# Kernel optimization log

Hardware: AMD Instinct MI355X
Metric: run time of the kernel (lower is better)

## Reference

```python
import jax, jax.numpy as jnp
import numpy as np

EPS = 1e-5  # torch LayerNorm default


def setup_inputs() -> dict:
    key = jax.random.key(0)
    ks = jax.random.split(key, 4)
    B, S, D = 8, 1024, 768
    return {
        "q": jax.random.normal(ks[0], (B, S, D), dtype=jnp.float32),
        "k": jax.random.normal(ks[1], (B, S, D), dtype=jnp.float32),
        "v": jax.random.normal(ks[2], (B, S, D), dtype=jnp.float32),
        "W": jax.random.normal(ks[3], (D, D), dtype=jnp.float32) * (1.0 / np.sqrt(D)),
        "gamma": jnp.ones((D,), dtype=jnp.float32),
        "beta": jnp.zeros((D,), dtype=jnp.float32),
        "n_heads": 12,
    }


def reference(q, k, v, W, gamma, beta, n_heads):
    # Shapes: q,k,v [B,S,D]; W [D,D] (torch Linear weight, y = x @ W.T)
    B, S, D = q.shape
    Dh = D // n_heads

    proj = lambda x: jax.nn.relu(x @ W.T)
    q1, k1, v1 = proj(q), proj(k), proj(v)

    # chunk(dim=2) + cat(dim=0) == reshape to per-head [B,S,H,Dh]
    split = lambda x: x.reshape(B, S, n_heads, Dh)
    qh, kh, vh = split(q1), split(k1), split(v1)

    scale = 1.0 / (Dh ** 0.5)
    scores = jnp.einsum("bqhd,bkhd->bhqk", qh, kh) * scale  # [B,H,S,S]
    attn = jax.nn.softmax(scores, axis=-1)  # dropout is identity in eval mode
    out = jnp.einsum("bhqk,bkhd->bqhd", attn, vh).reshape(B, S, D)

    # `outputs += outputs + q` in torch -> outputs = 2*outputs + q
    out = 2.0 * out + q

    mu = jnp.mean(out, axis=-1, keepdims=True)
    var = jnp.var(out, axis=-1, keepdims=True)
    return (out - mu) / jnp.sqrt(var + EPS) * gamma + beta
```

## Files before the change

kernel.cpp:

```cpp
#include <hip/hip_runtime.h>
#include <hip/hip_bf16.h>

#define B_  8
#define S_  1024
#define D_  768
#define H_  12
#define DH_ 64

typedef __attribute__((ext_vector_type(8))) short bf16x8;
typedef __attribute__((ext_vector_type(4))) float f32x4;
typedef __attribute__((ext_vector_type(16))) float f32x16;

__device__ inline short f2bf(float f) {
    unsigned u = __builtin_bit_cast(unsigned, f);
    u = (u + 0x7fffu + ((u >> 16) & 1u)) >> 16;
    return (short)u;
}
__device__ inline float exp2_fast(float x) {
    float r; asm("v_exp_f32 %0, %1" : "=v"(r) : "v"(x)); return r;
}
__device__ inline unsigned cvt_pk_bf16(float lo, float hi) {
    unsigned r; asm("v_cvt_pk_bf16_f32 %0, %1, %2" : "=v"(r) : "v"(lo), "v"(hi)); return r;
}
__device__ inline float rcp_fast(float x) {
    float r; asm("v_rcp_f32 %0, %1" : "=v"(r) : "v"(x)); return r;
}
__device__ inline void plswap(unsigned& a, unsigned& b) {
    auto r = __builtin_amdgcn_permlane32_swap(a, b, false, false);
    a = r[0]; b = r[1];
}
__device__ inline float2 xhalves(float x) {
    unsigned u = __builtin_bit_cast(unsigned, x);
    auto r = __builtin_amdgcn_permlane32_swap(u, u, false, false);
    return make_float2(__builtin_bit_cast(float, r[0]),
                       __builtin_bit_cast(float, r[1]));
}

__global__ __launch_bounds__(256) void proj_kernel(
    const float* __restrict__ q, const float* __restrict__ k,
    const float* __restrict__ v, const float* __restrict__ W,
    short* __restrict__ q1, short* __restrict__ k1, short* __restrict__ v1t)
{
    __shared__ __align__(16) char lds_raw[36864];
    short (*As)[72]  = reinterpret_cast<short(*)[72]>(lds_raw);
    short (*Bs)[72]  = reinterpret_cast<short(*)[72]>(lds_raw + 18432);
    short (*Ts)[136] = reinterpret_cast<short(*)[136]>(lds_raw);

    int p  = blockIdx.x;
    int L  = (p & 7) * 144 + (p >> 3);
    int mt = L / 6, nt = L % 6;
    int t  = mt >> 6;
    int m0 = (mt & 63) << 7;
    int n0 = nt << 7;
    const float* X = (t == 0) ? q : (t == 1) ? k : v;

    int tid  = threadIdx.x;
    int lane = tid & 63;
    int w    = tid >> 6;
    int wr   = w >> 1, wc = w & 1;
    int l15  = lane & 15;
    int g    = lane >> 4;

    int srow = tid >> 4;
    int scol = (tid & 15) << 2;

    const float* ax = X + (size_t)(m0 + srow) * D_ + scol;
    const float* bx = W + (size_t)(n0 + srow) * D_ + scol;

    f32x4 acc[4][4];
    #pragma unroll
    for (int m = 0; m < 4; m++)
        #pragma unroll
        for (int n = 0; n < 4; n++) acc[m][n] = (f32x4){0.f, 0.f, 0.f, 0.f};

    f32x4 la[8], lb[8];
    #pragma unroll
    for (int r = 0; r < 8; r++) {
        la[r] = *(const f32x4*)(ax + r * 16 * D_);
        lb[r] = *(const f32x4*)(bx + r * 16 * D_);
    }

    for (int kb = 0; kb < D_; kb += 64) {
        asm volatile("" ::: "memory");
        __builtin_amdgcn_s_barrier();
        asm volatile("" ::: "memory");
        #pragma unroll
        for (int r = 0; r < 8; r++) {
            uint2 ua, ub;
            ua.x = cvt_pk_bf16(la[r][0], la[r][1]);
            ua.y = cvt_pk_bf16(la[r][2], la[r][3]);
            ub.x = cvt_pk_bf16(lb[r][0], lb[r][1]);
            ub.y = cvt_pk_bf16(lb[r][2], lb[r][3]);
            *(uint2*)&As[r * 16 + srow][scol] = ua;
            *(uint2*)&Bs[r * 16 + srow][scol] = ub;
        }
        if (kb + 64 < D_) {
            #pragma unroll
            for (int r = 0; r < 8; r++) {
                la[r] = *(const f32x4*)(ax + kb + 64 + r * 16 * D_);
                lb[r] = *(const f32x4*)(bx + kb + 64 + r * 16 * D_);
            }
        }
        asm volatile("s_waitcnt lgkmcnt(0)" ::: "memory");
        __builtin_amdgcn_s_barrier();
        __builtin_amdgcn_sched_barrier(0);
        #pragma unroll
        for (int kk = 0; kk < 2; kk++) {
            int c = kk * 32 + (g << 3);
            bf16x8 af[4], bfv[4];
            #pragma unroll
            for (int m = 0; m < 4; m++)
                af[m] = *(const bf16x8*)&As[wr * 64 + m * 16 + l15][c];
            #pragma unroll
            for (int n = 0; n < 4; n++)
                bfv[n] = *(const bf16x8*)&Bs[wc * 64 + n * 16 + l15][c];
            #pragma unroll
            for (int m = 0; m < 4; m++)
                #pragma unroll
                for (int n = 0; n < 4; n++)
                    acc[m][n] = __builtin_amdgcn_mfma_f32_16x16x32_bf16(
                        af[m], bfv[n], acc[m][n], 0, 0, 0);
        }
    }

    __syncthreads();
    const float sc1 = (t == 1) ? 0.18033688011112793f : 1.0f;
    #pragma unroll
    for (int m = 0; m < 4; m++) {
        int rb = wr * 64 + m * 16 + (g << 2);
        #pragma unroll
        for (int n = 0; n < 4; n++) {
            int cb = wc * 64 + n * 16 + l15;
            #pragma unroll
            for (int r = 0; r < 4; r++) {
                short vv = f2bf(fmaxf(acc[m][n][r], 0.f) * sc1);
                if (t == 2) Ts[cb][rb + r] = vv;
                else        Ts[rb + r][cb] = vv;
            }
        }
    }
    __syncthreads();
    int row = tid >> 1;
    int c0  = (tid & 1) << 6;
    if (t == 2) {
        int gc = n0 + row;
        int h = gc >> 6, dh = gc & 63;
        int bb = m0 >> 10, s0 = m0 & 1023;
        short* dst = v1t + (((size_t)bb * H_ + h) * DH_ + dh) * S_ + s0 + c0;
        #pragma unroll
        for (int j = 0; j < 8; j++)
            *(bf16x8*)(dst + j * 8) = *(const bf16x8*)&Ts[row][c0 + j * 8];
    } else {
        int m = m0 + row;
        int bb = m >> 10, ss = m & 1023;
        int h = (n0 >> 6) + (tid & 1);
        short* dst = (t ? k1 : q1) + (((size_t)bb * H_ + h) * S_ + ss) * DH_;
        #pragma unroll
        for (int j = 0; j < 8; j++)
            *(bf16x8*)(dst + j * 8) = *(const bf16x8*)&Ts[row][c0 + j * 8];
    }
}

__global__ __launch_bounds__(256, 3) void attn_kernel(
    const short* __restrict__ q1, const short* __restrict__ k1,
    const short* __restrict__ v1t, float* __restrict__ out)
{
    __shared__ short Klds[2][4096];
    __shared__ short Vlds[2][4096];
    __shared__ float lsum_lds[4][32];

    int d    = blockIdx.x;
    int head = (d & 7) + ((d >> 6) << 3);
    int qi   = (d >> 3) & 7;
    int bb   = head / H_, hh = head % H_;

    int tid = threadIdx.x, lane = tid & 63, w = tid >> 6;
    int l31 = lane & 31, hi = lane >> 5;
    int qbase = (qi * 4 + w) * 32;

    const short* Qp = q1  + (size_t)head * S_ * DH_;
    const short* Kp = k1  + (size_t)head * S_ * DH_;
    const short* Vp = v1t + (size_t)head * DH_ * S_;

    int sr = tid >> 2, sc = tid & 3;
    int swz0 = sr * 128 + ((sc       ^ (sr & 7)) << 4);
    int swz1 = sr * 128 + (((sc + 4) ^ (sr & 7)) << 4);

    bf16x8 stK0, stK1, stV0, stV1;

#define LOADST(kvb) do { \
        const short* _kg = Kp + (size_t)((kvb) + sr) * DH_; \
        const short* _vg = Vp + (size_t)sr * S_ + (kvb); \
        stK0 = *(const bf16x8*)(_kg + sc * 8); \
        stK1 = *(const bf16x8*)(_kg + (sc + 4) * 8); \
        stV0 = *(const bf16x8*)(_vg + sc * 8); \
        stV1 = *(const bf16x8*)(_vg + (sc + 4) * 8); \
    } while (0)
#define WRITEST(buf) do { \
        char* _kb = (char*)&Klds[buf][0]; \
        char* _vb = (char*)&Vlds[buf][0]; \
        *(bf16x8*)(_kb + swz0) = stK0; \
        *(bf16x8*)(_kb + swz1) = stK1; \
        *(bf16x8*)(_vb + swz0) = stV0; \
        *(bf16x8*)(_vb + swz1) = stV1; \
    } while (0)

    bf16x8 qf[4];
    #pragma unroll
    for (int kb = 0; kb < 4; kb++)
        qf[kb] = *(const bf16x8*)(Qp + (size_t)(qbase + l31) * DH_ + kb * 16 + hi * 8);

    f32x16 o0, o1;
    #pragma unroll
    for (int r = 0; r < 16; r++) { o0[r] = 0.f; o1[r] = 0.f; }
    float mreg = -1e30f, lsum = 0.f;

    int xk = l31 & 7;

    auto subtile = [&](int cur, int j) {
        const char* Kt = (const char*)&Klds[cur][0];
        const char* Vt = (const char*)&Vlds[cur][0];
        int rK = (32 * j + l31) * 128;
        bf16x8 kf0 = *(const bf16x8*)(Kt + rK + (((0 + hi) ^ xk) << 4));
        bf16x8 kf1 = *(const bf16x8*)(Kt + rK + (((2 + hi) ^ xk) << 4));
        bf16x8 kf2 = *(const bf16x8*)(Kt + rK + (((4 + hi) ^ xk) << 4));
        bf16x8 kf3 = *(const bf16x8*)(Kt + rK + (((6 + hi) ^ xk) << 4));
        int rV0 = l31 * 128, rV1 = (32 + l31) * 128;
        int s0 = ((4 * j + hi) ^ xk) << 4, s1 = ((4 * j + 2 + hi) ^ xk) << 4;
        bf16x8 vf00 = *(const bf16x8*)(Vt + rV0 + s0);
        bf16x8 vf01 = *(const bf16x8*)(Vt + rV0 + s1);
        bf16x8 vf10 = *(const bf16x8*)(Vt + rV1 + s0);
        bf16x8 vf11 = *(const bf16x8*)(Vt + rV1 + s1);

        f32x16 s;
        #pragma unroll
        for (int r = 0; r < 16; r++) s[r] = 0.f;
        __builtin_amdgcn_s_setprio(1);
        s = __builtin_amdgcn_mfma_f32_32x32x16_bf16(kf0, qf[0], s, 0, 0, 0);
        s = __builtin_amdgcn_mfma_f32_32x32x16_bf16(kf1, qf[1], s, 0, 0, 0);
        s = __builtin_amdgcn_mfma_f32_32x32x16_bf16(kf2, qf[2], s, 0, 0, 0);
        s = __builtin_amdgcn_mfma_f32_32x32x16_bf16(kf3, qf[3], s, 0, 0, 0);
        __builtin_amdgcn_s_setprio(0);

        float t0 = fmaxf(s[0], s[1]),   t1 = fmaxf(s[2], s[3]);
        float t2 = fmaxf(s[4], s[5]),   t3 = fmaxf(s[6], s[7]);
        float t4 = fmaxf(s[8], s[9]),   t5 = fmaxf(s[10], s[11]);
        float t6 = fmaxf(s[12], s[13]), t7 = fmaxf(s[14], s[15]);
        float u0 = fmaxf(t0, t1), u1 = fmaxf(t2, t3);
        float u2 = fmaxf(t4, t5), u3 = fmaxf(t6, t7);
        float pmax = fmaxf(fmaxf(u0, u1), fmaxf(u2, u3));
        float2 ph = xhalves(pmax);
        pmax = fmaxf(ph.x, ph.y);

        if (!__all(pmax <= mreg + 8.f)) {
            float mn = fmaxf(mreg, pmax);
            float sc_ = exp2_fast(mreg - mn);
            mreg = mn; lsum *= sc_;
            if (hi == 0) lsum_lds[w][l31] = sc_;
            asm volatile("s_waitcnt lgkmcnt(0)" ::: "memory");
            #pragma unroll
            for (int r = 0; r < 16; r++) {
                int crow = (r & 3) + ((r >> 2) << 3) + (hi << 2);
                float srw = lsum_lds[w][crow];
                o0[r] *= srw; o1[r] *= srw;
            }
        }

        #pragma unroll
        for (int r = 0; r < 16; r++) s[r] = exp2_fast(s[r] - mreg);

        float a0 = s[0] + s[1],   a1 = s[2] + s[3];
        float a2 = s[4] + s[5],   a3 = s[6] + s[7];
        float a4 = s[8] + s[9],   a5 = s[10] + s[11];
        float a6 = s[12] + s[13], a7 = s[14] + s[15];
        float rsum = ((a0 + a1) + (a2 + a3)) + ((a4 + a5) + (a6 + a7));
        float2 rh = xhalves(rsum);
        lsum += rh.x + rh.y;

        unsigned c0 = cvt_pk_bf16(s[0], s[1]);
        unsigned c1 = cvt_pk_bf16(s[2], s[3]);
        unsigned c2 = cvt_pk_bf16(s[4], s[5]);
        unsigned c3 = cvt_pk_bf16(s[6], s[7]);
        unsigned c4 = cvt_pk_bf16(s[8], s[9]);
        unsigned c5 = cvt_pk_bf16(s[10], s[11]);
        unsigned c6 = cvt_pk_bf16(s[12], s[13]);
        unsigned c7 = cvt_pk_bf16(s[14], s[15]);
        plswap(c0, c2);
        plswap(c1, c3);
        plswap(c4, c6);
        plswap(c5, c7);

        union U { unsigned u[4]; bf16x8 v; };
        U f0, f1;
        f0.u[0] = c0; f0.u[1] = c1; f0.u[2] = c2; f0.u[3] = c3;
        f1.u[0] = c4; f1.u[1] = c5; f1.u[2] = c6; f1.u[3] = c7;

        __builtin_amdgcn_s_setprio(1);
        o0 = __builtin_amdgcn_mfma_f32_32x32x16_bf16(f0.v, vf00, o0, 0, 0, 0);
        o0 = __builtin_amdgcn_mfma_f32_32x32x16_bf16(f1.v, vf01, o0, 0, 0, 0);
        o1 = __builtin_amdgcn_mfma_f32_32x32x16_bf16(f0.v, vf10, o1, 0, 0, 0);
        o1 = __builtin_amdgcn_mfma_f32_32x32x16_bf16(f1.v, vf11, o1, 0, 0, 0);
        __builtin_amdgcn_s_setprio(0);
    };

    LOADST(0);
    WRITEST(0);
    LOADST(64);
    asm volatile("s_waitcnt lgkmcnt(0)" ::: "memory");
    __builtin_amdgcn_s_barrier();
    asm volatile("" ::: "memory");

    int cur = 0;
    for (int t = 0; t < 16; t++) {
        if (t < 15) {
            WRITEST(cur ^ 1);
            if (t < 14) LOADST((t + 2) * 64);
        }
        subtile(cur, 0);
        subtile(cur, 1);
        if (t < 15) {
            asm volatile("" ::: "memory");
            asm volatile("s_waitcnt lgkmcnt(0)" ::: "memory");
            __builtin_amdgcn_s_barrier();
            asm volatile("" ::: "memory");
        }
        cur ^= 1;
    }
#undef LOADST
#undef WRITEST

    if (hi == 0) lsum_lds[w][l31] = lsum;
    asm volatile("s_waitcnt lgkmcnt(0)" ::: "memory");
    #pragma unroll
    for (int r = 0; r < 16; r++) {
        int crow = (r & 3) + ((r >> 2) << 3) + (hi << 2);
        float inv = rcp_fast(lsum_lds[w][crow]);
        float* op = out + ((size_t)(bb * S_ + qbase + crow)) * D_ + hh * DH_ + l31;
        op[0]  = o0[r] * inv;
        op[32] = o1[r] * inv;
    }
}

__global__ __launch_bounds__(192) void ln_kernel(
    const float* __restrict__ qin, const float* __restrict__ gamma,
    const float* __restrict__ beta, float* __restrict__ out)
{
    int row = blockIdx.x;
    int tid = threadIdx.x;
    size_t base = (size_t)row * D_ + tid * 4;

    f32x4 o  = *(const f32x4*)(out + base);
    f32x4 qv = *(const f32x4*)(qin + base);
    f32x4 x;
    float sum = 0.f, sq = 0.f;
    #pragma unroll
    for (int i = 0; i < 4; i++) {
        x[i] = 2.f * o[i] + qv[i];
        sum += x[i];
        sq  += x[i] * x[i];
    }
    #pragma unroll
    for (int msk = 1; msk < 64; msk <<= 1) {
        sum += __shfl_xor(sum, msk);
        sq  += __shfl_xor(sq, msk);
    }
    __shared__ float s1[3], s2[3];
    if ((tid & 63) == 0) { s1[tid >> 6] = sum; s2[tid >> 6] = sq; }
    __syncthreads();
    sum = s1[0] + s1[1] + s1[2];
    sq  = s2[0] + s2[1] + s2[2];
    float mu   = sum * (1.f / D_);
    float var  = sq * (1.f / D_) - mu * mu;
    float rstd = rsqrtf(var + 1e-5f);
    f32x4 g = *(const f32x4*)(gamma + tid * 4);
    f32x4 b = *(const f32x4*)(beta + tid * 4);
    f32x4 y;
    #pragma unroll
    for (int i = 0; i < 4; i++)
        y[i] = (x[i] - mu) * rstd * g[i] + b[i];
    *(f32x4*)(out + base) = y;
}

extern "C" void kernel_launch(void* const* d_in, const int* in_sizes, int n_in,
                              void* d_out, int out_size, void* d_ws, size_t ws_size,
                              hipStream_t stream)
{
    const float* q     = (const float*)d_in[0];
    const float* k     = (const float*)d_in[1];
    const float* v     = (const float*)d_in[2];
    const float* W     = (const float*)d_in[3];
    const float* gamma = (const float*)d_in[4];
    const float* beta  = (const float*)d_in[5];

    size_t per = (size_t)B_ * H_ * S_ * DH_;
    short* q1  = (short*)d_ws;
    short* k1  = q1 + per;
    short* v1t = k1 + per;
    float* out = (float*)d_out;

    proj_kernel<<<dim3(1152), dim3(256), 0, stream>>>(q, k, v, W, q1, k1, v1t);
    attn_kernel<<<dim3(768), dim3(256), 0, stream>>>(q1, k1, v1t, out);
    ln_kernel<<<dim3(B_ * S_), dim3(192), 0, stream>>>(q, gamma, beta, out);
}
```

Measured before the change: 120.7 us.

## Double-buffer projection GEMM LDS with XOR swizzle and finer K steps

Restructures the projection GEMM main loop into a double-buffered LDS pipeline over 32-wide K steps, so each iteration needs one barrier instead of two and the global loads run two steps ahead. Padded LDS rows are replaced with XOR-swizzled layouts for the A/B tiles and the epilogue transpose buffer to avoid bank conflicts, and total LDS drops to 32KB. The launch bound now asks for 4 blocks per CU, and MFMA sections get raised wave priority. The risks are register pressure from the occupancy hint and shallower per-step MFMA work relative to barrier overhead.

```diff
diff --git a/kernel.cpp b/kernel.cpp
--- a/kernel.cpp
+++ b/kernel.cpp
@@ -36,15 +36,12 @@
                        __builtin_bit_cast(float, r[1]));
 }
 
-__global__ __launch_bounds__(256) void proj_kernel(
+__global__ __launch_bounds__(256, 4) void proj_kernel(
     const float* __restrict__ q, const float* __restrict__ k,
     const float* __restrict__ v, const float* __restrict__ W,
     short* __restrict__ q1, short* __restrict__ k1, short* __restrict__ v1t)
 {
-    __shared__ __align__(16) char lds_raw[36864];
-    short (*As)[72]  = reinterpret_cast<short(*)[72]>(lds_raw);
-    short (*Bs)[72]  = reinterpret_cast<short(*)[72]>(lds_raw + 18432);
-    short (*Ts)[136] = reinterpret_cast<short(*)[136]>(lds_raw);
+    __shared__ __align__(16) char lds_raw[32768];
 
     int p  = blockIdx.x;
     int L  = (p & 7) * 144 + (p >> 3);
@@ -54,18 +51,40 @@
     int n0 = nt << 7;
     const float* X = (t == 0) ? q : (t == 1) ? k : v;
 
-    int tid  = threadIdx.x;
-    int lane = tid & 63;
-    int w    = tid >> 6;
-    int wr   = w >> 1, wc = w & 1;
-    int l15  = lane & 15;
-    int g    = lane >> 4;
-
-    int srow = tid >> 4;
-    int scol = (tid & 15) << 2;
-
-    const float* ax = X + (size_t)(m0 + srow) * D_ + scol;
-    const float* bx = W + (size_t)(n0 + srow) * D_ + scol;
+    int tid = threadIdx.x, lane = tid & 63, w = tid >> 6;
+    int wr = w >> 1, wc = w & 1;
+    int l15 = lane & 15, g = lane >> 4;
+
+    int srow = tid >> 1, h = tid & 1;
+    const float* ax = X + (size_t)(m0 + srow) * D_ + h * 16;
+    const float* bx = W + (size_t)(n0 + srow) * D_ + h * 16;
+
+    int wb0 = srow * 64 + ((((h << 1) | 0) ^ (srow & 3)) << 4);
+    int wb1 = srow * 64 + ((((h << 1) | 1) ^ (srow & 3)) << 4);
+    int fs = (g ^ (l15 & 3)) << 4;
+
+    f32x4 la[4], lb[4];
+#define LOADAB(step) do { int _c = (step) * 32; \
+        la[0] = *(const f32x4*)(ax + _c);      la[1] = *(const f32x4*)(ax + _c + 4); \
+        la[2] = *(const f32x4*)(ax + _c + 8);  la[3] = *(const f32x4*)(ax + _c + 12); \
+        lb[0] = *(const f32x4*)(bx + _c);      lb[1] = *(const f32x4*)(bx + _c + 4); \
+        lb[2] = *(const f32x4*)(bx + _c + 8);  lb[3] = *(const f32x4*)(bx + _c + 12); \
+    } while (0)
+#define CONVW(bufbase) do { \
+        uint4 ua0, ua1, ub0, ub1; \
+        ua0.x = cvt_pk_bf16(la[0][0], la[0][1]); ua0.y = cvt_pk_bf16(la[0][2], la[0][3]); \
+        ua0.z = cvt_pk_bf16(la[1][0], la[1][1]); ua0.w = cvt_pk_bf16(la[1][2], la[1][3]); \
+        ua1.x = cvt_pk_bf16(la[2][0], la[2][1]); ua1.y = cvt_pk_bf16(la[2][2], la[2][3]); \
+        ua1.z = cvt_pk_bf16(la[3][0], la[3][1]); ua1.w = cvt_pk_bf16(la[3][2], la[3][3]); \
+        ub0.x = cvt_pk_bf16(lb[0][0], lb[0][1]); ub0.y = cvt_pk_bf16(lb[0][2], lb[0][3]); \
+        ub0.z = cvt_pk_bf16(lb[1][0], lb[1][1]); ub0.w = cvt_pk_bf16(lb[1][2], lb[1][3]); \
+        ub1.x = cvt_pk_bf16(lb[2][0], lb[2][1]); ub1.y = cvt_pk_bf16(lb[2][2], lb[2][3]); \
+        ub1.z = cvt_pk_bf16(lb[3][0], lb[3][1]); ub1.w = cvt_pk_bf16(lb[3][2], lb[3][3]); \
+        *(uint4*)(lds_raw + (bufbase) + wb0)        = ua0; \
+        *(uint4*)(lds_raw + (bufbase) + wb1)        = ua1; \
+        *(uint4*)(lds_raw + (bufbase) + 8192 + wb0) = ub0; \
+        *(uint4*)(lds_raw + (bufbase) + 8192 + wb1) = ub1; \
+    } while (0)
 
     f32x4 acc[4][4];
     #pragma unroll
@@ -73,55 +92,41 @@
         #pragma unroll
         for (int n = 0; n < 4; n++) acc[m][n] = (f32x4){0.f, 0.f, 0.f, 0.f};
 
-    f32x4 la[8], lb[8];
-    #pragma unroll
-    for (int r = 0; r < 8; r++) {
-        la[r] = *(const f32x4*)(ax + r * 16 * D_);
-        lb[r] = *(const f32x4*)(bx + r * 16 * D_);
-    }
-
-    for (int kb = 0; kb < D_; kb += 64) {
-        asm volatile("" ::: "memory");
-        __builtin_amdgcn_s_barrier();
-        asm volatile("" ::: "memory");
-        #pragma unroll
-        for (int r = 0; r < 8; r++) {
-            uint2 ua, ub;
-            ua.x = cvt_pk_bf16(la[r][0], la[r][1]);
-            ua.y = cvt_pk_bf16(la[r][2], la[r][3]);
-            ub.x = cvt_pk_bf16(lb[r][0], lb[r][1]);
-            ub.y = cvt_pk_bf16(lb[r][2], lb[r][3]);
-            *(uint2*)&As[r * 16 + srow][scol] = ua;
-            *(uint2*)&Bs[r * 16 + srow][scol] = ub;
-        }
-        if (kb + 64 < D_) {
-            #pragma unroll
-            for (int r = 0; r < 8; r++) {
-                la[r] = *(const f32x4*)(ax + kb + 64 + r * 16 * D_);
-                lb[r] = *(const f32x4*)(bx + kb + 64 + r * 16 * D_);
-            }
-        }
-        asm volatile("s_waitcnt lgkmcnt(0)" ::: "memory");
-        __builtin_amdgcn_s_barrier();
-        __builtin_amdgcn_sched_barrier(0);
-        #pragma unroll
-        for (int kk = 0; kk < 2; kk++) {
-            int c = kk * 32 + (g << 3);
-            bf16x8 af[4], bfv[4];
-            #pragma unroll
-            for (int m = 0; m < 4; m++)
-                af[m] = *(const bf16x8*)&As[wr * 64 + m * 16 + l15][c];
+    LOADAB(0);
+    CONVW(0);
+    LOADAB(1);
+    asm volatile("s_waitcnt lgkmcnt(0)" ::: "memory");
+    __builtin_amdgcn_s_barrier();
+    asm volatile("" ::: "memory");
+
+    #pragma unroll 2
+    for (int s = 0; s < 24; ++s) {
+        if (s < 23) CONVW(((s + 1) & 1) << 14);
+        if (s < 22) LOADAB(s + 2);
+        const char* bufp = lds_raw + ((s & 1) << 14);
+        bf16x8 af[4], bfv[4];
+        #pragma unroll
+        for (int m = 0; m < 4; m++)
+            af[m] = *(const bf16x8*)(bufp + (wr * 64 + m * 16 + l15) * 64 + fs);
+        #pragma unroll
+        for (int n = 0; n < 4; n++)
+            bfv[n] = *(const bf16x8*)(bufp + 8192 + (wc * 64 + n * 16 + l15) * 64 + fs);
+        __builtin_amdgcn_s_setprio(1);
+        #pragma unroll
+        for (int m = 0; m < 4; m++)
             #pragma unroll
             for (int n = 0; n < 4; n++)
-                bfv[n] = *(const bf16x8*)&Bs[wc * 64 + n * 16 + l15][c];
-            #pragma unroll
-            for (int m = 0; m < 4; m++)
-                #pragma unroll
-                for (int n = 0; n < 4; n++)
-                    acc[m][n] = __builtin_amdgcn_mfma_f32_16x16x32_bf16(
-                        af[m], bfv[n], acc[m][n], 0, 0, 0);
+                acc[m][n] = __builtin_amdgcn_mfma_f32_16x16x32_bf16(
+                    af[m], bfv[n], acc[m][n], 0, 0, 0);
+        __builtin_amdgcn_s_setprio(0);
+        if (s < 23) {
+            asm volatile("s_waitcnt lgkmcnt(0)" ::: "memory");
+            __builtin_amdgcn_s_barrier();
+            asm volatile("" ::: "memory");
         }
     }
+#undef LOADAB
+#undef CONVW
 
     __syncthreads();
     const float sc1 = (t == 1) ? 0.18033688011112793f : 1.0f;
@@ -134,30 +139,35 @@
             #pragma unroll
             for (int r = 0; r < 4; r++) {
                 short vv = f2bf(fmaxf(acc[m][n][r], 0.f) * sc1);
-                if (t == 2) Ts[cb][rb + r] = vv;
-                else        Ts[rb + r][cb] = vv;
+                int rr = (t == 2) ? cb : rb + r;
+                int cc = (t == 2) ? rb + r : cb;
+                *(short*)(lds_raw + rr * 256 + (((cc >> 3) ^ (rr & 15)) << 4)
+                          + ((cc & 7) << 1)) = vv;
             }
         }
     }
     __syncthreads();
     int row = tid >> 1;
     int c0  = (tid & 1) << 6;
+    bf16x8 ov[8];
+    #pragma unroll
+    for (int j = 0; j < 8; j++)
+        ov[j] = *(const bf16x8*)(lds_raw + row * 256 +
+                 ((((c0 >> 3) + j) ^ (row & 15)) << 4));
     if (t == 2) {
         int gc = n0 + row;
-        int h = gc >> 6, dh = gc & 63;
+        int hh2 = gc >> 6, dh = gc & 63;
         int bb = m0 >> 10, s0 = m0 & 1023;
-        short* dst = v1t + (((size_t)bb * H_ + h) * DH_ + dh) * S_ + s0 + c0;
-        #pragma unroll
-        for (int j = 0; j < 8; j++)
-            *(bf16x8*)(dst + j * 8) = *(const bf16x8*)&Ts[row][c0 + j * 8];
+        short* dst = v1t + (((size_t)bb * H_ + hh2) * DH_ + dh) * S_ + s0 + c0;
+        #pragma unroll
+        for (int j = 0; j < 8; j++) *(bf16x8*)(dst + j * 8) = ov[j];
     } else {
         int m = m0 + row;
         int bb = m >> 10, ss = m & 1023;
-        int h = (n0 >> 6) + (tid & 1);
-        short* dst = (t ? k1 : q1) + (((size_t)bb * H_ + h) * S_ + ss) * DH_;
-        #pragma unroll
-        for (int j = 0; j < 8; j++)
-            *(bf16x8*)(dst + j * 8) = *(const bf16x8*)&Ts[row][c0 + j * 8];
+        int hh2 = (n0 >> 6) + (tid & 1);
+        short* dst = (t ? k1 : q1) + (((size_t)bb * H_ + hh2) * S_ + ss) * DH_;
+        #pragma unroll
+        for (int j = 0; j < 8; j++) *(bf16x8*)(dst + j * 8) = ov[j];
     }
 }
 
```

After: 232.9 us. +93.0%, slower.
